# Kernel optimization log

Hardware: AMD Instinct MI355X
Metric: run time of the kernel (lower is better)

The kernel has to match this reference:

```python
import jax, jax.numpy as jnp
import numpy as np

B, N, DIM = 8, 8192, 256
K, CDIM = 4096, 1024
COMMIT = 0.25


def setup_inputs() -> dict:
    key = jax.random.key(0)
    ks = jax.random.split(key, 4)
    x = jax.random.normal(ks[0], (B, N, DIM), dtype=jnp.float32)
    ln_g = jnp.ones((DIM,), jnp.float32)
    ln_b = jnp.zeros((DIM,), jnp.float32)
    w_pre = jax.random.normal(ks[1], (DIM, CDIM), jnp.float32) / np.sqrt(DIM)
    b_pre = jnp.zeros((CDIM,), jnp.float32)
    embed = jax.random.normal(ks[2], (K, CDIM), jnp.float32)
    w_post = jax.random.normal(ks[3], (CDIM, DIM), jnp.float32) / np.sqrt(CDIM)
    b_post = jnp.zeros((DIM,), jnp.float32)
    return {"x": x, "ln_g": ln_g, "ln_b": ln_b, "w_pre": w_pre, "b_pre": b_pre,
            "embed": embed, "w_post": w_post, "b_post": b_post}


def reference(x, ln_g, ln_b, w_pre, b_pre, embed, w_post, b_post):
    # LayerNorm over last dim (eps=1e-5, torch default)
    mu = jnp.mean(x, axis=-1, keepdims=True)
    var = jnp.mean((x - mu) ** 2, axis=-1, keepdims=True)
    xn = (x - mu) * jax.lax.rsqrt(var + 1e-5) * ln_g + ln_b
    # GELU (exact, erf-based as in torch default) then Linear dim->codebook_dim
    z_e = jax.nn.gelu(xn, approximate=False) @ w_pre + b_pre  # (B,N,CDIM)
    flat = z_e.reshape(-1, CDIM)                              # (B*N, CDIM)
    # squared euclidean distances to codebook, argmin, gather
    z_sq = jnp.sum(flat * flat, axis=1, keepdims=True)        # (BN,1)
    e_sq = jnp.sum(embed * embed, axis=1)                     # (K,)
    dist = z_sq - 2.0 * (flat @ embed.T) + e_sq[None, :]      # (BN,K)
    indices = jnp.argmin(dist, axis=1)                        # (BN,)
    z_q = embed[indices]                                      # (BN,CDIM)
    # commitment loss (z_q detached)
    commit = COMMIT * jnp.mean((flat - jax.lax.stop_gradient(z_q)) ** 2)
    # straight-through estimator
    z_q_st = flat + jax.lax.stop_gradient(z_q - flat)
    z_q_st = z_q_st.reshape(B, N, CDIM)
    quantized = z_q_st @ w_post + b_post                      # (B,N,DIM)
    return quantized, indices.reshape(B, N), commit
```

## Files before the change

kernel.cpp:

```cpp
#include <hip/hip_runtime.h>

#define BN_ROWS 65536
#define DIMX 256
#define CDIM 1024
#define KCODES 4096
#define NSP 32
#define NSLOT 5
#define NENT 6
#define CMARG 12.0f
#define RMARG 12.0f
#define QS 24.0f
#define INV_S2 (1.0f / (QS * QS))
#define FLT_BIG 3.402823466e+38f

static const size_t OFF_ESQ   = 0;
static const size_t OFF_IDXF  = 16384;
static const size_t OFF_CROW  = 278528;
static const size_t OFF_EPOST = 540672;
static const size_t OFF_EI8   = 4734976;
static const size_t OFF_NFLAG = 8929280;
static const size_t OFF_FLAG  = 8929344;
static const size_t OFF_CAND  = 9191488;

typedef __attribute__((ext_vector_type(4))) int i32x4;

#define GLOAD_LDS16(gsrc, ldst)                                                \
  __builtin_amdgcn_global_load_lds(                                            \
      (const __attribute__((address_space(1))) void*)(gsrc),                   \
      (__attribute__((address_space(3))) void*)(ldst), 16, 0, 0)

__device__ inline char q8(float f) {
  return (char)__float2int_rn(fminf(fmaxf(f * QS, -127.f), 127.f));
}
__device__ inline unsigned fkey(float s) {
  unsigned b = __float_as_uint(s);
  return b ^ ((unsigned)((int)b >> 31) | 0x80000000u);
}
__device__ inline float keyinv(unsigned k) {
  unsigned b = (k & 0x80000000u) ? (k ^ 0x80000000u) : ~k;
  return __uint_as_float(b);
}

__global__ __launch_bounds__(256) void k_esq(const float* __restrict__ embed,
                                             float* __restrict__ e_sq) {
  const int t = threadIdx.x, wv = t >> 6, lane = t & 63;
  const int row = blockIdx.x * 4 + wv;
  const float* e = embed + (size_t)row * CDIM;
  float s = 0.f;
  for (int k = lane * 4; k < CDIM; k += 256) {
    float4 v = *(const float4*)(e + k);
    s = fmaf(v.x, v.x, s); s = fmaf(v.y, v.y, s);
    s = fmaf(v.z, v.z, s); s = fmaf(v.w, v.w, s);
  }
#pragma unroll
  for (int o = 32; o > 0; o >>= 1) s += __shfl_xor(s, o);
  if (lane == 0) e_sq[row] = s;
}

__global__ __launch_bounds__(256) void k_ei8(const float* __restrict__ embed,
                                             char* __restrict__ Ei8) {
  const int t = threadIdx.x;
  const size_t row = blockIdx.x;
  float4 v = *(const float4*)(embed + row * CDIM + t * 4);
  *(char4*)(Ei8 + row * CDIM + t * 4) =
      make_char4(q8(v.x), q8(v.y), q8(v.z), q8(v.w));
}

__global__ __launch_bounds__(256) void k_ln_gelu_gemm(
    const float* __restrict__ x, const float* __restrict__ ln_g,
    const float* __restrict__ ln_b, const float* __restrict__ w_pre,
    const float* __restrict__ b_pre, float* __restrict__ zf,
    char* __restrict__ zi8, int row0) {
  __shared__ float g[16][DIMX];
  const int t = threadIdx.x;
  const int lrow0 = blockIdx.x * 16;
  const int grow0 = row0 + lrow0;
  const int wv = t >> 6, lane = t & 63;
#pragma unroll
  for (int j = 0; j < 4; ++j) {
    const int r = wv * 4 + j;
    const float* xr = x + (size_t)(grow0 + r) * DIMX;
    float4 v = *(const float4*)(xr + lane * 4);
    float s = v.x + v.y + v.z + v.w;
    float ss = v.x * v.x + v.y * v.y + v.z * v.z + v.w * v.w;
#pragma unroll
    for (int o = 32; o > 0; o >>= 1) { s += __shfl_xor(s, o); ss += __shfl_xor(ss, o); }
    const float mu = s * (1.0f / 256.0f);
    const float var = ss * (1.0f / 256.0f) - mu * mu;
    const float rstd = rsqrtf(var + 1e-5f);
    float vv[4] = {v.x, v.y, v.z, v.w};
#pragma unroll
    for (int q = 0; q < 4; ++q) {
      const int d = lane * 4 + q;
      float xn = (vv[q] - mu) * rstd * ln_g[d] + ln_b[d];
      g[r][d] = 0.5f * xn * (1.0f + erff(xn * 0.70710678118654752f));
    }
  }
  __syncthreads();
  float acc[16][4];
#pragma unroll
  for (int r = 0; r < 16; ++r)
#pragma unroll
    for (int c = 0; c < 4; ++c) acc[r][c] = 0.f;
#pragma unroll 2
  for (int d0 = 0; d0 < DIMX; d0 += 4) {
    float4 w0 = *(const float4*)(w_pre + (size_t)(d0 + 0) * CDIM + t * 4);
    float4 w1 = *(const float4*)(w_pre + (size_t)(d0 + 1) * CDIM + t * 4);
    float4 w2 = *(const float4*)(w_pre + (size_t)(d0 + 2) * CDIM + t * 4);
    float4 w3 = *(const float4*)(w_pre + (size_t)(d0 + 3) * CDIM + t * 4);
#pragma unroll
    for (int r = 0; r < 16; ++r) {
      float4 gv = *(const float4*)&g[r][d0];
      acc[r][0] = fmaf(gv.x, w0.x, acc[r][0]);
      acc[r][1] = fmaf(gv.x, w0.y, acc[r][1]);
      acc[r][2] = fmaf(gv.x, w0.z, acc[r][2]);
      acc[r][3] = fmaf(gv.x, w0.w, acc[r][3]);
      acc[r][0] = fmaf(gv.y, w1.x, acc[r][0]);
      acc[r][1] = fmaf(gv.y, w1.y, acc[r][1]);
      acc[r][2] = fmaf(gv.y, w1.z, acc[r][2]);
      acc[r][3] = fmaf(gv.y, w1.w, acc[r][3]);
      acc[r][0] = fmaf(gv.z, w2.x, acc[r][0]);
      acc[r][1] = fmaf(gv.z, w2.y, acc[r][1]);
      acc[r][2] = fmaf(gv.z, w2.z, acc[r][2]);
      acc[r][3] = fmaf(gv.z, w2.w, acc[r][3]);
      acc[r][0] = fmaf(gv.w, w3.x, acc[r][0]);
      acc[r][1] = fmaf(gv.w, w3.y, acc[r][1]);
      acc[r][2] = fmaf(gv.w, w3.z, acc[r][2]);
      acc[r][3] = fmaf(gv.w, w3.w, acc[r][3]);
    }
  }
  float4 bp = *(const float4*)(b_pre + t * 4);
#pragma unroll
  for (int r = 0; r < 16; ++r) {
    float4 o;
    o.x = acc[r][0] + bp.x; o.y = acc[r][1] + bp.y;
    o.z = acc[r][2] + bp.z; o.w = acc[r][3] + bp.w;
    *(float4*)(zf + (size_t)(lrow0 + r) * CDIM + t * 4) = o;
    *(char4*)(zi8 + (size_t)(lrow0 + r) * CDIM + t * 4) =
        make_char4(q8(o.x), q8(o.y), q8(o.z), q8(o.w));
  }
}

__global__ __launch_bounds__(256, 3) void k_score(
    const char* __restrict__ Ei8, const char* __restrict__ Zi8,
    const float* __restrict__ e_sq, uint2* __restrict__ cand, int chunk) {
  __shared__ __align__(16) char lds[2][16384];
  const int t = threadIdx.x;
  const int cpx = gridDim.x >> 3;
  const int bx = (blockIdx.x & 7) * cpx + (blockIdx.x >> 3);
  const int zblk = bx >> 5, csp = bx & 31;
  const int wid = t >> 6, l = t & 63;
  const int wr = wid >> 1, wc = wid & 1;
  const int lg = l >> 4, lo16 = l & 15;
  const int rowbase = zblk * 128;
  const int m0 = csp * 128;
  const int wr4 = wr * 4, wc4 = wc * 4, l16 = l * 16;

  const bool isA = (wid < 2);
  const int q = wid & 1;
  const char* sarr = isA ? Ei8 : Zi8;
  const int sbase = isA ? m0 : rowbase;
  const char* sp0 = sarr + (size_t)(sbase + q * 64 + lo16) * 1024 + lg * 16;
  const int dstbase = (isA ? 0 : 8192) + q * 4096;

  i32x4 acc[4][4];
#pragma unroll
  for (int mi = 0; mi < 4; ++mi)
#pragma unroll
    for (int ni = 0; ni < 4; ++ni) acc[mi][ni] = (i32x4){0, 0, 0, 0};

  {
    char* D = &lds[0][dstbase];
#pragma unroll
    for (int u = 0; u < 4; ++u) GLOAD_LDS16(sp0 + u * 16384, D + u * 1024);
  }

  for (int kt = 0; kt < 16; ++kt) {
    const char* Lc = lds[kt & 1];
    asm volatile("s_waitcnt vmcnt(0)" ::: "memory");
    __builtin_amdgcn_s_barrier();
    __builtin_amdgcn_sched_barrier(0);
    if (kt < 15) {
      char* Dst = &lds[(kt + 1) & 1][dstbase];
      const char* spk = sp0 + (kt + 1) * 64;
#pragma unroll
      for (int u = 0; u < 4; ++u) GLOAD_LDS16(spk + u * 16384, Dst + u * 1024);
    }
    i32x4 bh[4], a[4];
#pragma unroll
    for (int ni = 0; ni < 4; ++ni)
      bh[ni] = *(const i32x4*)(Lc + 8192 + (wc4 + ni) * 1024 + l16);
#pragma unroll
    for (int u = 0; u < 4; ++u)
      a[u] = *(const i32x4*)(Lc + (wr4 + u) * 1024 + l16);
    asm volatile("s_waitcnt lgkmcnt(0)" ::: "memory");
    __builtin_amdgcn_sched_barrier(0);
    __builtin_amdgcn_s_setprio(1);
#pragma unroll
    for (int u = 0; u < 4; ++u)
#pragma unroll
      for (int ni = 0; ni < 4; ++ni)
        acc[u][ni] = __builtin_amdgcn_mfma_i32_16x16x64_i8(a[u], bh[ni],
                                                           acc[u][ni], 0, 0, 0);
    __builtin_amdgcn_s_setprio(0);
  }

  float s1[4];
  int i1[4];
#pragma unroll
  for (int i = 0; i < 4; ++i) { s1[i] = FLT_BIG; i1[i] = 0x7fffffff; }
#pragma unroll
  for (int mi = 0; mi < 4; ++mi) {
    const int c0 = m0 + wr * 64 + mi * 16 + lg * 4;
    float4 es = *(const float4*)(e_sq + c0);
    float esv[4] = {es.x, es.y, es.z, es.w};
#pragma unroll
    for (int ni = 0; ni < 4; ++ni) {
#pragma unroll
      for (int j = 0; j < 4; ++j) {
        const float s = fmaf(-2.0f * INV_S2, (float)acc[mi][ni][j], esv[j]);
        const int c = c0 + j;
        if (s < s1[ni] || (s == s1[ni] && c < i1[ni])) { s1[ni] = s; i1[ni] = c; }
      }
    }
  }

  unsigned long long* red = (unsigned long long*)&lds[0][0];
  float* sb = (float*)&lds[0][2048];
  unsigned* sbi = (unsigned*)&lds[0][2560];
  unsigned* cnt = (unsigned*)&lds[0][3072];
  uint2* slot = (uint2*)&lds[0][3584];

  __syncthreads();
#pragma unroll
  for (int ni = 0; ni < 4; ++ni) {
    unsigned long long k1v =
        (((unsigned long long)fkey(s1[ni])) << 32) | (unsigned)i1[ni];
    unsigned long long o1 = __shfl_xor(k1v, 16);
    k1v = o1 < k1v ? o1 : k1v;
    o1 = __shfl_xor(k1v, 32);
    k1v = o1 < k1v ? o1 : k1v;
    if (lg == 0) {
      const int r = wc * 64 + ni * 16 + lo16;
      red[r * 2 + wr] = k1v;
    }
  }
  __syncthreads();
  if (t < 128) {
    unsigned long long a1 = red[t * 2 + 0], b1 = red[t * 2 + 1];
    if (b1 < a1) a1 = b1;
    sb[t] = keyinv((unsigned)(a1 >> 32));
    sbi[t] = (unsigned)(a1 & 0xFFFFFFFFull);
    cnt[t] = 0;
  }
  __syncthreads();
#pragma unroll
  for (int mi = 0; mi < 4; ++mi) {
    const int c0 = m0 + wr * 64 + mi * 16 + lg * 4;
    float4 es = *(const float4*)(e_sq + c0);
    float esv[4] = {es.x, es.y, es.z, es.w};
#pragma unroll
    for (int ni = 0; ni < 4; ++ni) {
      const int r = wc * 64 + ni * 16 + lo16;
      const float thr = sb[r] + CMARG;
#pragma unroll
      for (int j = 0; j < 4; ++j) {
        const float s = fmaf(-2.0f * INV_S2, (float)acc[mi][ni][j], esv[j]);
        const unsigned c = (unsigned)(c0 + j);
        if (s < thr && c != sbi[r]) {
          unsigned pos = atomicAdd(&cnt[r], 1u);
          if (pos < NSLOT)
            slot[r * NSLOT + pos] = make_uint2(__float_as_uint(s), c);
        }
      }
    }
  }
  __syncthreads();
  if (t < 128) {
    uint2* g = cand + (size_t)(rowbase + t) * (NSP * NENT) + csp * NENT;
    const unsigned ov = (cnt[t] > NSLOT) ? 0x40000000u : 0u;
    g[0] = make_uint2(__float_as_uint(sb[t]), sbi[t] | ov);
    const unsigned n = cnt[t] > NSLOT ? NSLOT : cnt[t];
#pragma unroll
    for (int k = 0; k < NSLOT; ++k)
      g[1 + k] = (k < (int)n) ? slot[t * NSLOT + k]
                              : make_uint2(__float_as_uint(FLT_BIG), 0xFFFFFFFFu);
  }
}

__global__ __launch_bounds__(256) void k_refine(
    const uint2* __restrict__ cand, const float* __restrict__ zf,
    const float* __restrict__ embed, int* __restrict__ idxf,
    float* __restrict__ crow, float* __restrict__ out_idx,
    int* __restrict__ flag_rows, int* __restrict__ nflag, int chunk,
    int row0) {
  const int t = threadIdx.x, wid = t >> 6, l = t & 63;
  const int lrow = blockIdx.x * 4 + wid;
  if (lrow >= chunk) return;
  const int grow = row0 + lrow;
  const uint2* base = cand + (size_t)lrow * (NSP * NENT);
  const uint2 e0 = base[l];
  const uint2 e1 = base[64 + l];
  const uint2 e2 = base[128 + l];
  const bool is0 = (l % NENT) == 0;
  const bool is1 = ((64 + l) % NENT) == 0;
  const bool is2 = ((128 + l) % NENT) == 0;
  float gm = FLT_BIG;
  if (is0) gm = fminf(gm, __uint_as_float(e0.x));
  if (is1) gm = fminf(gm, __uint_as_float(e1.x));
  if (is2) gm = fminf(gm, __uint_as_float(e2.x));
#pragma unroll
  for (int o = 32; o > 0; o >>= 1) gm = fminf(gm, __shfl_xor(gm, o));
  const float thr = gm + RMARG;
  bool myovf = (is0 && (e0.y & 0x40000000u) && __uint_as_float(e0.x) < thr) ||
               (is1 && (e1.y & 0x40000000u) && __uint_as_float(e1.x) < thr) ||
               (is2 && (e2.y & 0x40000000u) && __uint_as_float(e2.x) < thr);
  const bool ovf = __any(myovf);

  float zv[16];
#pragma unroll
  for (int j = 0; j < 16; ++j) zv[j] = zf[(size_t)lrow * CDIM + l + 64 * j];

  double d1 = 1e300;
  int i1 = 0x7fffffff;
#define PROC(E)                                                                \
  {                                                                            \
    const float sc_ = __uint_as_float(E.x);                                    \
    const int id_ = (int)(E.y & 0xFFFFu);                                      \
    unsigned long long mask = __ballot(sc_ < thr && id_ < KCODES);             \
    while (mask) {                                                             \
      const int src = __ffsll((unsigned long long)mask) - 1;                   \
      mask &= mask - 1;                                                        \
      const int c = __shfl(id_, src);                                          \
      const float* e = embed + (size_t)c * CDIM;                               \
      double dd = 0.0;                                                         \
      _Pragma("unroll") for (int j = 0; j < 16; ++j) {                         \
        const double df = (double)zv[j] - (double)e[l + 64 * j];               \
        dd = fma(df, df, dd);                                                  \
      }                                                                        \
      _Pragma("unroll") for (int o = 32; o > 0; o >>= 1) dd +=                 \
          __shfl_xor(dd, o);                                                   \
      if (dd < d1 || (dd == d1 && c < i1)) { d1 = dd; i1 = c; }                \
    }                                                                          \
  }
  PROC(e0);
  PROC(e1);
  PROC(e2);
#undef PROC
  if (l == 0) {
    idxf[grow] = i1;
    out_idx[grow] = (float)i1;
    crow[grow] = (float)d1;
    if (ovf) {
      const int s = atomicAdd(nflag, 1);
      flag_rows[s] = lrow;
    }
  }
}

__global__ __launch_bounds__(256) void k_exact(
    const float* __restrict__ zf, const float* __restrict__ embed,
    const int* __restrict__ flag_rows, const int* __restrict__ nflag,
    int* __restrict__ idxf, float* __restrict__ crow,
    float* __restrict__ out_idx, int row0) {
  __shared__ double wd[4];
  __shared__ int wcidx[4];
  const int t = threadIdx.x;
  const int wid = t >> 6, l = t & 63;
  const int n = *nflag;

  for (int fi = blockIdx.x; fi < n; fi += gridDim.x) {
    const int lrow = flag_rows[fi];
    const int grow = row0 + lrow;
    float zr[16];
#pragma unroll
    for (int j = 0; j < 16; ++j) zr[j] = zf[(size_t)lrow * CDIM + l + 64 * j];
    double dmin = 1e300;
    int cmin = 0x7fffffff;
    for (int ci = 0; ci < 1024; ++ci) {
      const int c = wid * 1024 + ci;
      const float* e = embed + (size_t)c * CDIM;
      double dd = 0.0;
#pragma unroll
      for (int j = 0; j < 16; ++j) {
        const double df = (double)zr[j] - (double)e[l + 64 * j];
        dd = fma(df, df, dd);
      }
#pragma unroll
      for (int o = 32; o > 0; o >>= 1) dd += __shfl_xor(dd, o);
      if (dd < dmin) { dmin = dd; cmin = c; }
    }
    if (l == 0) { wd[wid] = dmin; wcidx[wid] = cmin; }
    __syncthreads();
    if (t == 0) {
      double dm = wd[0]; int cm = wcidx[0];
#pragma unroll
      for (int wv = 1; wv < 4; ++wv) {
        if (wd[wv] < dm || (wd[wv] == dm && wcidx[wv] < cm)) {
          dm = wd[wv]; cm = wcidx[wv];
        }
      }
      idxf[grow] = cm;
      out_idx[grow] = (float)cm;
      crow[grow] = (float)dm;
    }
    __syncthreads();
  }
}

__global__ __launch_bounds__(256) void k_epost(const float* __restrict__ E,
                                               const float* __restrict__ w_post,
                                               float* __restrict__ E_post) {
  __shared__ float es[16][128];
  const int t = threadIdx.x;
  const int r0 = blockIdx.x * 16;
  float acc[16];
#pragma unroll
  for (int r = 0; r < 16; ++r) acc[r] = 0.f;
  for (int k0 = 0; k0 < CDIM; k0 += 128) {
    __syncthreads();
#pragma unroll
    for (int p = 0; p < 2; ++p) {
      const int fl = (p * 256 + t) * 4;
      const int r = fl >> 7, kk = fl & 127;
      float4 v = *(const float4*)(E + (size_t)(r0 + r) * CDIM + k0 + kk);
      *(float4*)&es[r][kk] = v;
    }
    __syncthreads();
#pragma unroll 4
    for (int d = 0; d < 128; ++d) {
      const float w = w_post[(size_t)(k0 + d) * DIMX + t];
#pragma unroll
      for (int r = 0; r < 16; ++r) acc[r] = fmaf(es[r][d], w, acc[r]);
    }
  }
#pragma unroll
  for (int r = 0; r < 16; ++r)
    E_post[(size_t)(r0 + r) * DIMX + t] = acc[r];
}

__global__ __launch_bounds__(256) void k_gather(const float* __restrict__ E_post,
                                                const int* __restrict__ idx,
                                                const float* __restrict__ b_post,
                                                float* __restrict__ outq) {
  const int t = threadIdx.x;
  const int r0 = blockIdx.x * 16;
  const float bp = b_post[t];
#pragma unroll
  for (int i = 0; i < 16; ++i) {
    const int row = r0 + i;
    outq[(size_t)row * DIMX + t] = E_post[(size_t)idx[row] * DIMX + t] + bp;
  }
}

__global__ __launch_bounds__(256) void k_commit_final(
    const float* __restrict__ crow, float* __restrict__ out_commit) {
  const int t = threadIdx.x;
  double s = 0.0;
  for (int i = t; i < BN_ROWS; i += 256) s += (double)crow[i];
#pragma unroll
  for (int o = 32; o > 0; o >>= 1) s += __shfl_xor(s, o);
  __shared__ double wsum[4];
  if ((t & 63) == 0) wsum[t >> 6] = s;
  __syncthreads();
  if (t == 0)
    *out_commit = (float)(0.25 * (wsum[0] + wsum[1] + wsum[2] + wsum[3]) /
                          (65536.0 * 1024.0));
}

extern "C" void kernel_launch(void* const* d_in, const int* in_sizes, int n_in,
                              void* d_out, int out_size, void* d_ws,
                              size_t ws_size, hipStream_t stream) {
  const float* x = (const float*)d_in[0];
  const float* ln_g = (const float*)d_in[1];
  const float* ln_b = (const float*)d_in[2];
  const float* w_pre = (const float*)d_in[3];
  const float* b_pre = (const float*)d_in[4];
  const float* embed = (const float*)d_in[5];
  const float* w_post = (const float*)d_in[6];
  const float* b_post = (const float*)d_in[7];

  float* out = (float*)d_out;
  float* outq = out;
  float* out_idx = out + 16777216;
  float* out_commit = out + 16842752;

  char* ws = (char*)d_ws;
  float* e_sq = (float*)(ws + OFF_ESQ);
  int* idxf = (int*)(ws + OFF_IDXF);
  float* crow = (float*)(ws + OFF_CROW);
  float* E_post = (float*)(ws + OFF_EPOST);
  char* Ei8 = (char*)(ws + OFF_EI8);
  int* nflag = (int*)(ws + OFF_NFLAG);
  int* flag_rows = (int*)(ws + OFF_FLAG);

  int chunk = 4096;
  while (chunk < BN_ROWS &&
         OFF_CAND + (size_t)(chunk * 2) * 6656ull <= ws_size)
    chunk *= 2;
  uint2* cand = (uint2*)(ws + OFF_CAND);
  char* zi8 = ws + OFF_CAND + (size_t)chunk * 1536;
  float* zf = (float*)(ws + OFF_CAND + (size_t)chunk * 1536 +
                       (size_t)chunk * 1024);

  k_esq<<<KCODES / 4, 256, 0, stream>>>(embed, e_sq);
  k_ei8<<<KCODES, 256, 0, stream>>>(embed, Ei8);
  k_epost<<<KCODES / 16, 256, 0, stream>>>(embed, w_post, E_post);

  for (int row0 = 0; row0 < BN_ROWS; row0 += chunk) {
    hipMemsetAsync(nflag, 0, sizeof(int), stream);
    k_ln_gelu_gemm<<<chunk / 16, 256, 0, stream>>>(x, ln_g, ln_b, w_pre, b_pre,
                                                   zf, zi8, row0);
    k_score<<<(chunk / 128) * NSP, 256, 0, stream>>>(Ei8, zi8, e_sq, cand,
                                                     chunk);
    k_refine<<<chunk / 4, 256, 0, stream>>>(cand, zf, embed, idxf, crow,
                                            out_idx, flag_rows, nflag, chunk,
                                            row0);
    k_exact<<<128, 256, 0, stream>>>(zf, embed, flag_rows, nflag, idxf, crow,
                                     out_idx, row0);
  }

  k_gather<<<BN_ROWS / 16, 256, 0, stream>>>(E_post, idxf, b_post, outq);
  k_commit_final<<<1, 256, 0, stream>>>(crow, out_commit);
}
```

Before: 1.411 ms.

## Load int8 score operands directly from global into registers, dropping LDS staging

```diff
diff --git a/kernel.cpp b/kernel.cpp
--- a/kernel.cpp
+++ b/kernel.cpp
@@ -23,11 +23,6 @@
 static const size_t OFF_CAND  = 9191488;
 
 typedef __attribute__((ext_vector_type(4))) int i32x4;
-
-#define GLOAD_LDS16(gsrc, ldst)                                                \
-  __builtin_amdgcn_global_load_lds(                                            \
-      (const __attribute__((address_space(1))) void*)(gsrc),                   \
-      (__attribute__((address_space(3))) void*)(ldst), 16, 0, 0)
 
 __device__ inline char q8(float f) {
   return (char)__float2int_rn(fminf(fmaxf(f * QS, -127.f), 127.f));
@@ -144,7 +139,7 @@
 __global__ __launch_bounds__(256, 3) void k_score(
     const char* __restrict__ Ei8, const char* __restrict__ Zi8,
     const float* __restrict__ e_sq, uint2* __restrict__ cand, int chunk) {
-  __shared__ __align__(16) char lds[2][16384];
+  __shared__ __align__(16) char lds[16384];
   const int t = threadIdx.x;
   const int cpx = gridDim.x >> 3;
   const int bx = (blockIdx.x & 7) * cpx + (blockIdx.x >> 3);
@@ -154,14 +149,9 @@
   const int lg = l >> 4, lo16 = l & 15;
   const int rowbase = zblk * 128;
   const int m0 = csp * 128;
-  const int wr4 = wr * 4, wc4 = wc * 4, l16 = l * 16;
-
-  const bool isA = (wid < 2);
-  const int q = wid & 1;
-  const char* sarr = isA ? Ei8 : Zi8;
-  const int sbase = isA ? m0 : rowbase;
-  const char* sp0 = sarr + (size_t)(sbase + q * 64 + lo16) * 1024 + lg * 16;
-  const int dstbase = (isA ? 0 : 8192) + q * 4096;
+
+  const char* pa = Ei8 + (size_t)(m0 + wr * 64 + lo16) * 1024 + lg * 16;
+  const char* pb = Zi8 + (size_t)(rowbase + wc * 64 + lo16) * 1024 + lg * 16;
 
   i32x4 acc[4][4];
 #pragma unroll
@@ -169,40 +159,39 @@
 #pragma unroll
     for (int ni = 0; ni < 4; ++ni) acc[mi][ni] = (i32x4){0, 0, 0, 0};
 
-  {
-    char* D = &lds[0][dstbase];
-#pragma unroll
-    for (int u = 0; u < 4; ++u) GLOAD_LDS16(sp0 + u * 16384, D + u * 1024);
-  }
-
-  for (int kt = 0; kt < 16; ++kt) {
-    const char* Lc = lds[kt & 1];
-    asm volatile("s_waitcnt vmcnt(0)" ::: "memory");
-    __builtin_amdgcn_s_barrier();
-    __builtin_amdgcn_sched_barrier(0);
-    if (kt < 15) {
-      char* Dst = &lds[(kt + 1) & 1][dstbase];
-      const char* spk = sp0 + (kt + 1) * 64;
-#pragma unroll
-      for (int u = 0; u < 4; ++u) GLOAD_LDS16(spk + u * 16384, Dst + u * 1024);
-    }
-    i32x4 bh[4], a[4];
-#pragma unroll
-    for (int ni = 0; ni < 4; ++ni)
-      bh[ni] = *(const i32x4*)(Lc + 8192 + (wc4 + ni) * 1024 + l16);
+  i32x4 aA[4], bA[4], aB[4], bB[4];
+#pragma unroll
+  for (int u = 0; u < 4; ++u) {
+    aA[u] = *(const i32x4*)(pa + u * 16384);
+    bA[u] = *(const i32x4*)(pb + u * 16384);
+  }
+#pragma unroll
+  for (int kt2 = 0; kt2 < 8; ++kt2) {
+    const int kt = kt2 * 2;
+#pragma unroll
+    for (int u = 0; u < 4; ++u) {
+      aB[u] = *(const i32x4*)(pa + u * 16384 + (kt + 1) * 64);
+      bB[u] = *(const i32x4*)(pb + u * 16384 + (kt + 1) * 64);
+    }
 #pragma unroll
     for (int u = 0; u < 4; ++u)
-      a[u] = *(const i32x4*)(Lc + (wr4 + u) * 1024 + l16);
-    asm volatile("s_waitcnt lgkmcnt(0)" ::: "memory");
-    __builtin_amdgcn_sched_barrier(0);
-    __builtin_amdgcn_s_setprio(1);
+#pragma unroll
+      for (int ni = 0; ni < 4; ++ni)
+        acc[u][ni] = __builtin_amdgcn_mfma_i32_16x16x64_i8(aA[u], bA[ni],
+                                                           acc[u][ni], 0, 0, 0);
+    if (kt + 2 < 16) {
+#pragma unroll
+      for (int u = 0; u < 4; ++u) {
+        aA[u] = *(const i32x4*)(pa + u * 16384 + (kt + 2) * 64);
+        bA[u] = *(const i32x4*)(pb + u * 16384 + (kt + 2) * 64);
+      }
+    }
 #pragma unroll
     for (int u = 0; u < 4; ++u)
 #pragma unroll
       for (int ni = 0; ni < 4; ++ni)
-        acc[u][ni] = __builtin_amdgcn_mfma_i32_16x16x64_i8(a[u], bh[ni],
+        acc[u][ni] = __builtin_amdgcn_mfma_i32_16x16x64_i8(aB[u], bB[ni],
                                                            acc[u][ni], 0, 0, 0);
-    __builtin_amdgcn_s_setprio(0);
   }
 
   float s1[4];
@@ -225,11 +214,11 @@
     }
   }
 
-  unsigned long long* red = (unsigned long long*)&lds[0][0];
-  float* sb = (float*)&lds[0][2048];
-  unsigned* sbi = (unsigned*)&lds[0][2560];
-  unsigned* cnt = (unsigned*)&lds[0][3072];
-  uint2* slot = (uint2*)&lds[0][3584];
+  unsigned long long* red = (unsigned long long*)&lds[0];
+  float* sb = (float*)&lds[2048];
+  unsigned* sbi = (unsigned*)&lds[2560];
+  unsigned* cnt = (unsigned*)&lds[3072];
+  uint2* slot = (uint2*)&lds[3584];
 
   __syncthreads();
 #pragma unroll
```

Measured after the change: 1.864 ms. 32.1% more time.
